# Optimization experiments

Hardware: AMD Instinct MI355X
Metric: run time of the kernel (lower is better)

Reference implementation:

```python
import jax, jax.numpy as jnp
import numpy as np

B, L, C, OUT = 8, 256, 512, 512


def setup_inputs() -> dict:
    key = jax.random.key(0)
    ks = jax.random.split(key, 8)
    xd = jax.random.normal(ks[0], (B, L, C), jnp.float32)
    xt = jax.random.normal(ks[1], (B, L, C), jnp.float32)
    # Linear weights stored (in, out): y = x @ W + b (equiv. to torch x @ W^T)
    Wc = jax.random.normal(ks[2], (C, C), jnp.float32) * 0.02
    bc = jnp.zeros((C,), jnp.float32)
    Wp = jax.random.normal(ks[3], (C, C), jnp.float32) * 0.02
    bp = jnp.zeros((C,), jnp.float32)
    Wf = jax.random.normal(ks[4], (C, OUT), jnp.float32) * 0.02
    bf = jnp.zeros((OUT,), jnp.float32)
    return {"xd": xd, "xt": xt, "Wc": Wc, "bc": bc, "Wp": Wp, "bp": bp, "Wf": Wf, "bf": bf}


def reference(xd, xt, Wc, bc, Wp, bp, Wf, bf):
    # projected features
    pt = jax.nn.relu(xt) @ Wp + bp              # (b, Lt, C)
    pc = jax.nn.relu(xd) @ Wc + bc              # (b, Ld, C)
    # sigmoid bilinear scores: (b, Lt, Ld) == (b, Ld, Lt) since Lt == Ld structurally
    scores = jax.nn.sigmoid(jnp.einsum('bic,bkc->bik', pt, pc))
    # normalize by total per-batch sum
    w = scores / jnp.sum(scores, axis=(1, 2), keepdims=True)
    # tanh of elementwise outer product, reduced with attention weights
    # cp[b,c] = sum_{i,j} tanh(xd[b,i,c] * xt[b,j,c]) * w[b,i,j]
    cp = jnp.einsum('bijc,bij->bc', jnp.tanh(xd[:, :, None, :] * xt[:, None, :, :]), w)
    return cp @ Wf + bf
```

## Files before the change

### kernel.cpp

```cpp
#include <hip/hip_runtime.h>
#include <math.h>

#define B_   8
#define L_   256
#define C_   512
#define OUT_ 512

typedef _Float16 half8 __attribute__((ext_vector_type(8)));
typedef float    f32x4 __attribute__((ext_vector_type(4)));
typedef float    f32x2 __attribute__((ext_vector_type(2)));

__global__ __launch_bounds__(256)
void proj_mfma_kernel(const float* __restrict__ xt, const float* __restrict__ Wp,
                      const float* __restrict__ bp,
                      const float* __restrict__ xd, const float* __restrict__ Wc,
                      const float* __restrict__ bc,
                      _Float16* __restrict__ pt, _Float16* __restrict__ pc,
                      float* __restrict__ P)
{
    const int which = blockIdx.z;
    const float* __restrict__ X    = which ? xd : xt;
    const float* __restrict__ W    = which ? Wc : Wp;
    const float* __restrict__ bias = which ? bc : bp;
    _Float16*    __restrict__ Y    = which ? pc : pt;

    if (which == 0 && blockIdx.y == 0) {
        const int pb = (int)blockIdx.x << 9;
        P[pb | threadIdx.x]         = 0.f;
        P[pb | (threadIdx.x + 256)] = 0.f;
    }

    __shared__ _Float16 Ah[2][64][40];
    __shared__ _Float16 Bh[2][64][40];
    __shared__ _Float16 Ot[64][72];

    const int tid = threadIdx.x;
    const int m0 = blockIdx.y << 6, n0 = blockIdx.x << 6;
    const int lane = tid & 63, wv = tid >> 6;
    const int l15 = lane & 15, quad = lane >> 4;

    const int srow = tid >> 2, sch = (tid & 3) << 3;
    const float* Ag = X + (size_t)(m0 + srow) * C_ + sch;
    const int nl = tid & 63, kseg = tid >> 6;
    const float* Bg = W + (size_t)(kseg << 3) * C_ + n0 + nl;

    float4 a0 = *(const float4*)(Ag);
    float4 a1 = *(const float4*)(Ag + 4);
    float wr[8];
    #pragma unroll
    for (int r = 0; r < 8; ++r) wr[r] = Bg[(size_t)r * C_];

    {
        half8 av;
        av[0] = (_Float16)fmaxf(a0.x, 0.f); av[1] = (_Float16)fmaxf(a0.y, 0.f);
        av[2] = (_Float16)fmaxf(a0.z, 0.f); av[3] = (_Float16)fmaxf(a0.w, 0.f);
        av[4] = (_Float16)fmaxf(a1.x, 0.f); av[5] = (_Float16)fmaxf(a1.y, 0.f);
        av[6] = (_Float16)fmaxf(a1.z, 0.f); av[7] = (_Float16)fmaxf(a1.w, 0.f);
        *(half8*)&Ah[0][srow][sch] = av;
        half8 bv;
        #pragma unroll
        for (int r = 0; r < 8; ++r) bv[r] = (_Float16)wr[r];
        *(half8*)&Bh[0][nl][kseg << 3] = bv;
    }

    f32x4 acc[4] = {};
    for (int ks = 0; ks < 16; ++ks) {
        const int cur = ks & 1;
        if (ks < 15) {
            Ag += 32;
            Bg += 32 * C_;
            a0 = *(const float4*)(Ag);
            a1 = *(const float4*)(Ag + 4);
            #pragma unroll
            for (int r = 0; r < 8; ++r) wr[r] = Bg[(size_t)r * C_];
        }
        __syncthreads();
        half8 af = *(const half8*)&Ah[cur][(wv << 4) + l15][quad << 3];
        #pragma unroll
        for (int nb = 0; nb < 4; ++nb) {
            half8 bf = *(const half8*)&Bh[cur][(nb << 4) + l15][quad << 3];
            acc[nb] = __builtin_amdgcn_mfma_f32_16x16x32_f16(af, bf, acc[nb], 0, 0, 0);
        }
        if (ks < 15) {
            half8 av;
            av[0] = (_Float16)fmaxf(a0.x, 0.f); av[1] = (_Float16)fmaxf(a0.y, 0.f);
            av[2] = (_Float16)fmaxf(a0.z, 0.f); av[3] = (_Float16)fmaxf(a0.w, 0.f);
            av[4] = (_Float16)fmaxf(a1.x, 0.f); av[5] = (_Float16)fmaxf(a1.y, 0.f);
            av[6] = (_Float16)fmaxf(a1.z, 0.f); av[7] = (_Float16)fmaxf(a1.w, 0.f);
            *(half8*)&Ah[cur ^ 1][srow][sch] = av;
            half8 bv;
            #pragma unroll
            for (int r = 0; r < 8; ++r) bv[r] = (_Float16)wr[r];
            *(half8*)&Bh[cur ^ 1][nl][kseg << 3] = bv;
        }
    }

    __syncthreads();
    #pragma unroll
    for (int nb = 0; nb < 4; ++nb) {
        const float bz = bias[n0 + (nb << 4) + l15];
        #pragma unroll
        for (int r = 0; r < 4; ++r)
            Ot[(wv << 4) + (quad << 2) + r][(nb << 4) + l15] = (_Float16)(acc[nb][r] + bz);
    }
    __syncthreads();
    const int erow = tid >> 3, ech = (tid & 7) << 3;
    #pragma unroll
    for (int h = 0; h < 64; h += 32)
        *(half8*)&Y[(size_t)(m0 + erow + h) * C_ + n0 + ech] = *(const half8*)&Ot[erow + h][ech];
}

__device__ __forceinline__ float sigmoid_fast(float z) {
    float e = __builtin_amdgcn_exp2f(-1.4426950408889634f * z);
    return __builtin_amdgcn_rcpf(e + 1.0f);
}

__global__ __launch_bounds__(512, 4)
void cp_scores_kernel(const _Float16* __restrict__ pt, const _Float16* __restrict__ pc,
                      const float* __restrict__ xd, const float* __restrict__ xt,
                      float* __restrict__ P, float* __restrict__ sums_part)
{
    const int bx = blockIdx.x, by = blockIdx.y, b = blockIdx.z;
    const int i0 = bx << 5, j0 = by << 4;
    const int tid = threadIdx.x;
    const int lane = tid & 63, wv = tid >> 6;
    const int l15 = lane & 15, quad = lane >> 4;

    __shared__ _Float16 Ah[2][32][40];
    __shared__ _Float16 Bh[2][16][40];
    __shared__ float ws_[16][36];
    __shared__ float wred[2];

    const int srow = tid >> 2;
    const int sch  = (tid & 3) << 3;
    const _Float16* Sg = ((srow < 32) ? pt + (size_t)(b * L_ + i0 + srow) * C_
                                      : pc + (size_t)(b * L_ + j0 + (srow - 32)) * C_) + sch;

    half8 v = {};
    if (tid < 192) {
        v = *(const half8*)Sg;
        if (srow < 32) *(half8*)&Ah[0][srow][sch] = v;
        else           *(half8*)&Bh[0][srow - 32][sch] = v;
    }

    f32x4 acc = {};
    for (int ks = 0; ks < 16; ++ks) {
        const int cur = ks & 1;
        if (ks < 15 && tid < 192) { Sg += 32; v = *(const half8*)Sg; }
        __syncthreads();
        if (wv < 2) {
            half8 af = *(const half8*)&Ah[cur][(wv << 4) + l15][quad << 3];
            half8 bf = *(const half8*)&Bh[cur][l15][quad << 3];
            acc = __builtin_amdgcn_mfma_f32_16x16x32_f16(af, bf, acc, 0, 0, 0);
        }
        if (ks < 15 && tid < 192) {
            if (srow < 32) *(half8*)&Ah[cur ^ 1][srow][sch] = v;
            else           *(half8*)&Bh[cur ^ 1][srow - 32][sch] = v;
        }
    }

    float lsum = 0.f;
    if (wv < 2) {
        float4 sg;
        sg.x = sigmoid_fast(acc[0]);
        sg.y = sigmoid_fast(acc[1]);
        sg.z = sigmoid_fast(acc[2]);
        sg.w = sigmoid_fast(acc[3]);
        *(float4*)&ws_[l15][(wv << 4) + (quad << 2)] = sg;
        lsum = (sg.x + sg.y) + (sg.z + sg.w);
    }
    #pragma unroll
    for (int off = 32; off; off >>= 1) lsum += __shfl_xor(lsum, off);
    if (wv < 2 && lane == 0) wred[wv] = lsum;
    __syncthreads();
    if (tid == 0)
        sums_part[(b << 7) | (bx << 4) | by] = wred[0] + wred[1];

    const int c = tid;
    const float* __restrict__ xdb = xd + (size_t)(b * L_ + i0) * C_ + c;
    const float* __restrict__ xtb = xt + (size_t)(b * L_ + j0) * C_ + c;

    float total = 0.f;
    #pragma unroll
    for (int ih = 0; ih < 2; ++ih) {
        f32x2 xds2[8];
        #pragma unroll
        for (int i = 0; i < 8; ++i) {
            xds2[i].x = xdb[(size_t)((ih << 4) + 2 * i) * C_]     * 2.8853900817779268f;
            xds2[i].y = xdb[(size_t)((ih << 4) + 2 * i + 1) * C_] * 2.8853900817779268f;
        }
        f32x2 A0 = {0.f, 0.f}, A1 = {0.f, 0.f}, A2 = {0.f, 0.f}, A3 = {0.f, 0.f};
        float xv = xtb[0];
        #pragma unroll 4
        for (int jj = 0; jj < 16; ++jj) {
            const float xv_n = (jj < 15) ? xtb[(size_t)(jj + 1) * C_] : 0.f;
            #pragma unroll
            for (int g = 0; g < 4; ++g) {
                const float4 w4 = *(const float4*)&ws_[jj][(ih << 4) + (g << 2)];
                const f32x2 xp0 = xds2[(g << 1)];
                const f32x2 xp1 = xds2[(g << 1) + 1];
                f32x2 x01 = xp0 * xv;
                f32x2 e01 = { __builtin_amdgcn_exp2f(x01.x), __builtin_amdgcn_exp2f(x01.y) };
                f32x2 q01 = e01 + 1.0f;
                float rp01 = __builtin_amdgcn_rcpf(q01.x * q01.y);
                f32x2 r01 = rp01 * __builtin_shufflevector(q01, q01, 1, 0);
                f32x2 w01 = { w4.x, w4.y };
                f32x2 x23 = xp1 * xv;
                f32x2 e23 = { __builtin_amdgcn_exp2f(x23.x), __builtin_amdgcn_exp2f(x23.y) };
                f32x2 q23 = e23 + 1.0f;
                float rp23 = __builtin_amdgcn_rcpf(q23.x * q23.y);
                f32x2 r23 = rp23 * __builtin_shufflevector(q23, q23, 1, 0);
                f32x2 w23 = { w4.z, w4.w };
                switch (g) {
                    case 0: A0 = w01 * r01 + A0; A1 = w23 * r23 + A1; break;
                    case 1: A2 = w01 * r01 + A2; A3 = w23 * r23 + A3; break;
                    case 2: A0 = w01 * r01 + A0; A1 = w23 * r23 + A1; break;
                    default: A2 = w01 * r01 + A2; A3 = w23 * r23 + A3; break;
                }
            }
            xv = xv_n;
        }
        total += ((A0.x + A0.y) + (A1.x + A1.y)) + ((A2.x + A2.y) + (A3.x + A3.y));
    }
    atomicAdd(&P[(b << 9) | c], total);
}

__global__ __launch_bounds__(256)
void finalize_kernel(const float* __restrict__ P, const float* __restrict__ sums_part,
                     const float* __restrict__ Wf, const float* __restrict__ bfv,
                     float* __restrict__ out)
{
    const int b = blockIdx.y;
    const int t = threadIdx.x;
    __shared__ float cp[C_];
    __shared__ float red[256];
    __shared__ float sumsh;

    red[t] = (t < 128) ? sums_part[(b << 7) | t] : 0.f;
    __syncthreads();
    for (int st = 64; st > 0; st >>= 1) {
        if (t < st) red[t] += red[t + st] + ((st == 64) ? red[t + 128] : 0.f);
        __syncthreads();
    }
    if (t == 0) sumsh = red[0];
    __syncthreads();

    const float inv = 2.0f / sumsh;
    cp[t]       = 1.0f - P[(b << 9) | t] * inv;
    cp[t + 256] = 1.0f - P[(b << 9) | (t + 256)] * inv;
    __syncthreads();

    const int o     = ((int)blockIdx.x << 6) | (t & 63);
    const int cbase = (t >> 6) << 7;
    float acc = 0.f;
    #pragma unroll 8
    for (int i = 0; i < 128; ++i) {
        const int cc = cbase + i;
        acc = fmaf(cp[cc], Wf[(size_t)cc * OUT_ + o], acc);
    }
    red[t] = acc;
    __syncthreads();
    if (t < 64) {
        float a = ((red[t] + red[t + 64]) + (red[t + 128] + red[t + 192]));
        out[(size_t)b * OUT_ + o] = a + bfv[o];
    }
}

extern "C" void kernel_launch(void* const* d_in, const int* in_sizes, int n_in,
                              void* d_out, int out_size, void* d_ws, size_t ws_size,
                              hipStream_t stream)
{
    const float* xd = (const float*)d_in[0];
    const float* xt = (const float*)d_in[1];
    const float* Wc = (const float*)d_in[2];
    const float* bc = (const float*)d_in[3];
    const float* Wp = (const float*)d_in[4];
    const float* bp = (const float*)d_in[5];
    const float* Wf = (const float*)d_in[6];
    const float* bf = (const float*)d_in[7];
    float* out = (float*)d_out;

    _Float16* pt  = (_Float16*)d_ws;
    _Float16* pc  = pt + 1048576;
    float* P         = (float*)(pc + 1048576);
    float* sums_part = P + B_ * C_;

    proj_mfma_kernel<<<dim3(8, 32, 2), 256, 0, stream>>>(xt, Wp, bp, xd, Wc, bc, pt, pc, P);
    cp_scores_kernel<<<dim3(8, 16, 8), 512, 0, stream>>>(pt, pc, xd, xt, P, sums_part);
    finalize_kernel<<<dim3(8, 8), 256, 0, stream>>>(P, sums_part, Wf, bf, out);
}
```

Baseline: 140.9 us.

## Fuse finalize GEMV into scores kernel via last-block atomic counter

Removes the separate finalize launch. Each cp_scores block bumps a per-batch atomic counter, and the last block of each batch reduces the score sums, normalizes P and runs the 512x512 Wf GEMV in place. The inner tanh accumulation is also reworked into scalar FMA accumulators with a combined numerator, and the xt prefetch is dropped. This trades one kernel launch for a serialized tail GEMV done by only 8 blocks, plus an extra fence and atomic in every block.

```diff
diff --git a/kernel.cpp b/kernel.cpp
--- a/kernel.cpp
+++ b/kernel.cpp
@@ -16,7 +16,7 @@
                       const float* __restrict__ xd, const float* __restrict__ Wc,
                       const float* __restrict__ bc,
                       _Float16* __restrict__ pt, _Float16* __restrict__ pc,
-                      float* __restrict__ P)
+                      float* __restrict__ P, int* __restrict__ cnt)
 {
     const int which = blockIdx.z;
     const float* __restrict__ X    = which ? xd : xt;
@@ -28,6 +28,7 @@
         const int pb = (int)blockIdx.x << 9;
         P[pb | threadIdx.x]         = 0.f;
         P[pb | (threadIdx.x + 256)] = 0.f;
+        if (threadIdx.x == 0) cnt[blockIdx.x] = 0;
     }
 
     __shared__ _Float16 Ah[2][64][40];
@@ -118,7 +119,10 @@
 __global__ __launch_bounds__(512, 4)
 void cp_scores_kernel(const _Float16* __restrict__ pt, const _Float16* __restrict__ pc,
                       const float* __restrict__ xd, const float* __restrict__ xt,
-                      float* __restrict__ P, float* __restrict__ sums_part)
+                      float* __restrict__ P, float* __restrict__ sums_part,
+                      int* __restrict__ cnt,
+                      const float* __restrict__ Wf, const float* __restrict__ bfv,
+                      float* __restrict__ out)
 {
     const int bx = blockIdx.x, by = blockIdx.y, b = blockIdx.z;
     const int i0 = bx << 5, j0 = by << 4;
@@ -130,6 +134,9 @@
     __shared__ _Float16 Bh[2][16][40];
     __shared__ float ws_[16][36];
     __shared__ float wred[2];
+    __shared__ float sred[128];
+    __shared__ float cpsh[C_];
+    __shared__ int   lastFlag;
 
     const int srow = tid >> 2;
     const int sch  = (tid & 3) << 3;
@@ -143,7 +150,7 @@
         else           *(half8*)&Bh[0][srow - 32][sch] = v;
     }
 
-    f32x4 acc = {};
+    f32x4 dacc = {};
     for (int ks = 0; ks < 16; ++ks) {
         const int cur = ks & 1;
         if (ks < 15 && tid < 192) { Sg += 32; v = *(const half8*)Sg; }
@@ -151,7 +158,7 @@
         if (wv < 2) {
             half8 af = *(const half8*)&Ah[cur][(wv << 4) + l15][quad << 3];
             half8 bf = *(const half8*)&Bh[cur][l15][quad << 3];
-            acc = __builtin_amdgcn_mfma_f32_16x16x32_f16(af, bf, acc, 0, 0, 0);
+            dacc = __builtin_amdgcn_mfma_f32_16x16x32_f16(af, bf, dacc, 0, 0, 0);
         }
         if (ks < 15 && tid < 192) {
             if (srow < 32) *(half8*)&Ah[cur ^ 1][srow][sch] = v;
@@ -162,10 +169,10 @@
     float lsum = 0.f;
     if (wv < 2) {
         float4 sg;
-        sg.x = sigmoid_fast(acc[0]);
-        sg.y = sigmoid_fast(acc[1]);
-        sg.z = sigmoid_fast(acc[2]);
-        sg.w = sigmoid_fast(acc[3]);
+        sg.x = sigmoid_fast(dacc[0]);
+        sg.y = sigmoid_fast(dacc[1]);
+        sg.z = sigmoid_fast(dacc[2]);
+        sg.w = sigmoid_fast(dacc[3]);
         *(float4*)&ws_[l15][(wv << 4) + (quad << 2)] = sg;
         lsum = (sg.x + sg.y) + (sg.z + sg.w);
     }
@@ -186,84 +193,70 @@
         f32x2 xds2[8];
         #pragma unroll
         for (int i = 0; i < 8; ++i) {
-            xds2[i].x = xdb[(size_t)((ih << 4) + 2 * i) * C_]     * 2.8853900817779268f;
-            xds2[i].y = xdb[(size_t)((ih << 4) + 2 * i + 1) * C_] * 2.8853900817779268f;
-        }
-        f32x2 A0 = {0.f, 0.f}, A1 = {0.f, 0.f}, A2 = {0.f, 0.f}, A3 = {0.f, 0.f};
-        float xv = xtb[0];
-        #pragma unroll 4
+            xds2[i][0] = xdb[(size_t)((ih << 4) + 2 * i) * C_]     * 2.8853900817779268f;
+            xds2[i][1] = xdb[(size_t)((ih << 4) + 2 * i + 1) * C_] * 2.8853900817779268f;
+        }
+        float A0 = 0.f, A1 = 0.f, A2 = 0.f, A3 = 0.f;
+        #pragma unroll 2
         for (int jj = 0; jj < 16; ++jj) {
-            const float xv_n = (jj < 15) ? xtb[(size_t)(jj + 1) * C_] : 0.f;
+            const float xv = xtb[(size_t)jj * C_];
+            const f32x2 xvv = {xv, xv};
             #pragma unroll
             for (int g = 0; g < 4; ++g) {
                 const float4 w4 = *(const float4*)&ws_[jj][(ih << 4) + (g << 2)];
-                const f32x2 xp0 = xds2[(g << 1)];
-                const f32x2 xp1 = xds2[(g << 1) + 1];
-                f32x2 x01 = xp0 * xv;
-                f32x2 e01 = { __builtin_amdgcn_exp2f(x01.x), __builtin_amdgcn_exp2f(x01.y) };
-                f32x2 q01 = e01 + 1.0f;
-                float rp01 = __builtin_amdgcn_rcpf(q01.x * q01.y);
-                f32x2 r01 = rp01 * __builtin_shufflevector(q01, q01, 1, 0);
-                f32x2 w01 = { w4.x, w4.y };
-                f32x2 x23 = xp1 * xv;
-                f32x2 e23 = { __builtin_amdgcn_exp2f(x23.x), __builtin_amdgcn_exp2f(x23.y) };
-                f32x2 q23 = e23 + 1.0f;
-                float rp23 = __builtin_amdgcn_rcpf(q23.x * q23.y);
-                f32x2 r23 = rp23 * __builtin_shufflevector(q23, q23, 1, 0);
-                f32x2 w23 = { w4.z, w4.w };
-                switch (g) {
-                    case 0: A0 = w01 * r01 + A0; A1 = w23 * r23 + A1; break;
-                    case 1: A2 = w01 * r01 + A2; A3 = w23 * r23 + A3; break;
-                    case 2: A0 = w01 * r01 + A0; A1 = w23 * r23 + A1; break;
-                    default: A2 = w01 * r01 + A2; A3 = w23 * r23 + A3; break;
-                }
+                f32x2 x0 = xds2[(g << 1)]     * xvv;
+                f32x2 x1 = xds2[(g << 1) + 1] * xvv;
+                f32x2 e0 = { __builtin_amdgcn_exp2f(x0[0]), __builtin_amdgcn_exp2f(x0[1]) };
+                f32x2 e1 = { __builtin_amdgcn_exp2f(x1[0]), __builtin_amdgcn_exp2f(x1[1]) };
+                f32x2 q0 = e0 + 1.0f;
+                f32x2 q1 = e1 + 1.0f;
+                const float rp0 = __builtin_amdgcn_rcpf(q0[0] * q0[1]);
+                const float rp1 = __builtin_amdgcn_rcpf(q1[0] * q1[1]);
+                float t0 = w4.x * q0[1];
+                t0 = fmaf(w4.y, q0[0], t0);
+                float t1 = w4.z * q1[1];
+                t1 = fmaf(w4.w, q1[0], t1);
+                if (g & 1) { A2 = fmaf(t0, rp0, A2); A3 = fmaf(t1, rp1, A3); }
+                else       { A0 = fmaf(t0, rp0, A0); A1 = fmaf(t1, rp1, A1); }
             }
-            xv = xv_n;
-        }
-        total += ((A0.x + A0.y) + (A1.x + A1.y)) + ((A2.x + A2.y) + (A3.x + A3.y));
+        }
+        total += ((A0 + A1) + (A2 + A3));
     }
     atomicAdd(&P[(b << 9) | c], total);
-}
-
-__global__ __launch_bounds__(256)
-void finalize_kernel(const float* __restrict__ P, const float* __restrict__ sums_part,
-                     const float* __restrict__ Wf, const float* __restrict__ bfv,
-                     float* __restrict__ out)
-{
-    const int b = blockIdx.y;
-    const int t = threadIdx.x;
-    __shared__ float cp[C_];
-    __shared__ float red[256];
-    __shared__ float sumsh;
-
-    red[t] = (t < 128) ? sums_part[(b << 7) | t] : 0.f;
+
+    __threadfence();
+    __syncthreads();
+    if (tid == 0) {
+        int old = __hip_atomic_fetch_add(&cnt[b], 1, __ATOMIC_ACQ_REL,
+                                         __HIP_MEMORY_SCOPE_AGENT);
+        lastFlag = (old == 127);
+    }
+    __syncthreads();
+    if (!lastFlag) return;
+
+    __threadfence();
+    float sv = 0.f;
+    if (tid < 128)
+        sv = __hip_atomic_load(&sums_part[(b << 7) | tid], __ATOMIC_RELAXED,
+                               __HIP_MEMORY_SCOPE_AGENT);
+    if (tid < 128) sred[tid] = sv;
     __syncthreads();
     for (int st = 64; st > 0; st >>= 1) {
-        if (t < st) red[t] += red[t + st] + ((st == 64) ? red[t + 128] : 0.f);
+        if (tid < st) sred[tid] += sred[tid + st];
         __syncthreads();
     }
-    if (t == 0) sumsh = red[0];
-    __syncthreads();
-
-    const float inv = 2.0f / sumsh;
-    cp[t]       = 1.0f - P[(b << 9) | t] * inv;
-    cp[t + 256] = 1.0f - P[(b << 9) | (t + 256)] * inv;
-    __syncthreads();
-
-    const int o     = ((int)blockIdx.x << 6) | (t & 63);
-    const int cbase = (t >> 6) << 7;
-    float acc = 0.f;
+    const float invS = 2.0f / sred[0];
+
+    const float pv = __hip_atomic_load(&P[(b << 9) | tid], __ATOMIC_RELAXED,
+                                       __HIP_MEMORY_SCOPE_AGENT);
+    cpsh[tid] = 1.0f - pv * invS;
+    __syncthreads();
+
+    float oacc = bfv[tid];
     #pragma unroll 8
-    for (int i = 0; i < 128; ++i) {
-        const int cc = cbase + i;
-        acc = fmaf(cp[cc], Wf[(size_t)cc * OUT_ + o], acc);
-    }
-    red[t] = acc;
-    __syncthreads();
-    if (t < 64) {
-        float a = ((red[t] + red[t + 64]) + (red[t + 128] + red[t + 192]));
-        out[(size_t)b * OUT_ + o] = a + bfv[o];
-    }
+    for (int cc = 0; cc < C_; ++cc)
+        oacc = fmaf(cpsh[cc], Wf[(size_t)cc * OUT_ + tid], oacc);
+    out[(size_t)b * OUT_ + tid] = oacc;
 }
 
 extern "C" void kernel_launch(void* const* d_in, const int* in_sizes, int n_in,
@@ -284,8 +277,10 @@
     _Float16* pc  = pt + 1048576;
     float* P         = (float*)(pc + 1048576);
     float* sums_part = P + B_ * C_;
-
-    proj_mfma_kernel<<<dim3(8, 32, 2), 256, 0, stream>>>(xt, Wp, bp, xd, Wc, bc, pt, pc, P);
-    cp_scores_kernel<<<dim3(8, 16, 8), 512, 0, stream>>>(pt, pc, xd, xt, P, sums_part);
-    finalize_kernel<<<dim3(8, 8), 256, 0, stream>>>(P, sums_part, Wf, bf, out);
-}
+    int*   cnt       = (int*)(sums_part + 1024);
+
+    proj_mfma_kernel<<<dim3(8, 32, 2), 256, 0, stream>>>(xt, Wp, bp, xd, Wc, bc,
+                                                         pt, pc, P, cnt);
+    cp_scores_kernel<<<dim3(8, 16, 8), 512, 0, stream>>>(pt, pc, xd, xt, P, sums_part,
+                                                         cnt, Wf, bf, out);
+}
```

Result: slower. 332.7 us (+136.1%).
